# Optimization experiments

Measured on AMD Instinct MI355X. Metric: run time of the kernel, lower is better.

## Reference

```python
import jax, jax.numpy as jnp
import numpy as np

N_NODES = 1_000_000
N_EDGES = 5_000_000
N_GRAPHS = 4096
HIDDEN = 16


def transform(x):
    # Transform wrapper: fn=tanh, then nan_to_num(nan=0, posinf=10, neginf=-10).clamp(-10, 10)
    y = jnp.tanh(x)
    y = jnp.nan_to_num(y, nan=0.0, posinf=10.0, neginf=-10.0)
    return jnp.clip(y, -10.0, 10.0)


def setup_inputs() -> dict:
    key = jax.random.key(0)
    ks = jax.random.split(key, 10)
    x = jax.random.normal(ks[0], (N_NODES, 3), dtype=jnp.float32)
    edge_index = jax.random.randint(ks[1], (2, N_EDGES), 0, N_NODES, dtype=jnp.int32)
    batch = jnp.sort(jax.random.randint(ks[2], (N_NODES,), 0, N_GRAPHS, dtype=jnp.int32))
    s1 = 1.0 / np.sqrt(3.0)
    s2 = 1.0 / np.sqrt(HIDDEN)
    s3 = 1.0 / np.sqrt(2 * HIDDEN)
    w1 = jax.random.uniform(ks[3], (3, HIDDEN), jnp.float32, -s1, s1)
    b1 = jax.random.uniform(ks[4], (HIDDEN,), jnp.float32, -s1, s1)
    w2 = jax.random.uniform(ks[5], (HIDDEN, HIDDEN), jnp.float32, -s2, s2)
    b2 = jax.random.uniform(ks[6], (HIDDEN,), jnp.float32, -s2, s2)
    w3 = jax.random.uniform(ks[7], (2 * HIDDEN, 1), jnp.float32, -s3, s3)
    b3 = jax.random.uniform(ks[8], (1,), jnp.float32, -s3, s3)
    return {"x": x, "edge_index": edge_index, "batch": batch,
            "w1": w1, "b1": b1, "w2": w2, "b2": b2, "w3": w3, "b3": b3}


def reference(x, edge_index, batch, w1, b1, w2, b2, w3, b3):
    n_nodes = x.shape[0]
    h = transform(x @ w1 + b1)                                  # [N, H]
    row, col = edge_index[0], edge_index[1]
    # degree of each destination node (row), clamped to >= 1
    deg = jax.ops.segment_sum(jnp.ones((row.shape[0],), x.dtype), row,
                              num_segments=n_nodes)             # [N]
    deg = jnp.maximum(deg, 1.0)
    # gather source features, scatter-add to destinations, normalize
    agg = jax.ops.segment_sum(h[col], row, num_segments=n_nodes)  # [N, H]
    agg = agg / deg[:, None]
    h = transform(agg @ w2 + b2)                                # [N, H]
    # per-graph mean and max pooling
    cnt = jax.ops.segment_sum(jnp.ones((n_nodes,), x.dtype), batch,
                              num_segments=N_GRAPHS)            # [G]
    h_sum = jax.ops.segment_sum(h, batch, num_segments=N_GRAPHS)  # [G, H]
    h_mean = h_sum / jnp.maximum(cnt, 1.0)[:, None]
    h_max = jax.ops.segment_max(h, batch, num_segments=N_GRAPHS)  # [G, H]
    h_max = jnp.where(jnp.isneginf(h_max), 0.0, h_max)
    pooled = jnp.concatenate([h_mean, h_max], axis=1)           # [G, 2H]
    out = jax.nn.sigmoid(pooled @ w3 + b3)                      # [G, 1]
    return out.squeeze(-1)
```

## Files before the change

kernel.cpp:

```cpp
#include <hip/hip_runtime.h>
#include <hip/hip_bf16.h>
#include <hip/hip_fp16.h>

static constexpr int NN = 1000000;
static constexpr int NE = 5000000;
static constexpr int NG = 4096;
static constexpr int BIN_SH = 8;
static constexpr int BIN_SZ = 1 << BIN_SH;
static constexpr int NB = (NN + BIN_SZ - 1) >> BIN_SH;
static constexpr int CAP_SH = 11;
static constexpr int CAP = 1 << CAP_SH;
static constexpr int EPB = 16384;
static constexpr int BIN_BLOCKS = (NE + EPB - 1) / EPB;
static constexpr int CHUNK = 512;

__device__ __forceinline__ float fast_tanh(float x) {
    float e = __expf(2.0f * x);
    return 1.0f - 2.0f * __fdividef(1.0f, e + 1.0f);
}

__global__ __launch_bounds__(256) void x2h_k(
    const float* __restrict__ x, __half* __restrict__ xh)
{
    int i = blockIdx.x * 256 + threadIdx.x;
    if (i >= NN) return;
    union { __half2 h2[2]; uint2 u; } o;
    o.h2[0] = __floats2half2_rn(x[3 * i + 0], x[3 * i + 1]);
    o.h2[1] = __floats2half2_rn(x[3 * i + 2], 0.0f);
    *reinterpret_cast<uint2*>(xh + 4 * (size_t)i) = o.u;
}

__global__ __launch_bounds__(1024) void bin_scatter_k(
    const int* __restrict__ row, const int* __restrict__ col,
    int* __restrict__ binCursor, unsigned int* __restrict__ pack)
{
    __shared__ int hist[NB];
    for (int i = threadIdx.x; i < NB; i += 1024) hist[i] = 0;
    __syncthreads();
    int base = blockIdx.x * EPB;
#pragma unroll 4
    for (int k = 0; k < EPB / 1024; ++k) {
        int e = base + k * 1024 + threadIdx.x;
        if (e < NE) atomicAdd(&hist[row[e] >> BIN_SH], 1);
    }
    __syncthreads();
    for (int i = threadIdx.x; i < NB; i += 1024) {
        int c = hist[i];
        hist[i] = c ? ((i << CAP_SH) + atomicAdd(&binCursor[i], c)) : 0;
    }
    __syncthreads();
#pragma unroll 4
    for (int k = 0; k < EPB / 1024; ++k) {
        int e = base + k * 1024 + threadIdx.x;
        if (e >= NE) continue;
        int r = row[e];
        int c = col[e];
        int pos = atomicAdd(&hist[r >> BIN_SH], 1);
        pack[pos] = ((unsigned int)(r & (BIN_SZ - 1)) << 20) | (unsigned int)c;
    }
}

__global__ __launch_bounds__(256) void bucket_agg_k(
    const unsigned int* __restrict__ pack,
    const int* __restrict__ binCursor,
    const __half* __restrict__ xh,
    const int* __restrict__ batch,
    const float* __restrict__ w1,
    const float* __restrict__ b1,
    const float* __restrict__ w2,
    const float* __restrict__ b2,
    float* __restrict__ h_sum,
    unsigned int* __restrict__ h_max,
    int* __restrict__ cnt)
{
    __shared__ uint4 pay[CHUNK * 2];
    __shared__ int scnt[BIN_SZ];
    __shared__ int sstart[BIN_SZ];
    __shared__ int wsum[4];

    int tid = threadIdx.x;
    int lane = tid & 63, wid = tid >> 6;
    int b = blockIdx.x;
    int nodeBase = b << BIN_SH;
    int nNodes = min(BIN_SZ, NN - nodeBase);
    int es = b << CAP_SH;
    int ee = es + binCursor[b];

    __half2 acc8[8];
#pragma unroll
    for (int q = 0; q < 8; ++q) acc8[q] = __half2half2(__float2half(0.0f));
    int dg = 0;

    for (int cs = es; cs < ee; cs += CHUNK) {
        int m = min(CHUNK, ee - cs);
        scnt[tid] = 0;
        __syncthreads();

        uint2 gx[2];
        int rl2[2];
#pragma unroll
        for (int k = 0; k < 2; ++k) {
            int e = cs + k * 256 + tid;
            rl2[k] = -1;
            if (e < cs + m) {
                unsigned int p = pack[e];
                int c = (int)(p & 0xFFFFFu);
                rl2[k] = (int)(p >> 20);
                gx[k] = *reinterpret_cast<const uint2*>(xh + 4 * (size_t)c);
                atomicAdd(&scnt[rl2[k]], 1);
            }
        }
        __syncthreads();

        int v = scnt[tid];
        int sc = v;
#pragma unroll
        for (int off = 1; off < 64; off <<= 1) {
            int u = __shfl_up(sc, off);
            if (lane >= off) sc += u;
        }
        if (lane == 63) wsum[wid] = sc;
        __syncthreads();
        int pre = 0;
#pragma unroll
        for (int w = 0; w < 4; ++w) pre += (w < wid) ? wsum[w] : 0;
        int ex = pre + sc - v;
        sstart[tid] = ex;
        scnt[tid] = ex;
        __syncthreads();

#pragma unroll
        for (int k = 0; k < 2; ++k) {
            if (rl2[k] >= 0) {
                union { uint2 u; __half2 h2[2]; } xi;
                xi.u = gx[k];
                float2 x01 = __half22float2(xi.h2[0]);
                float x2v = __low2float(xi.h2[1]);
                union { __half2 h2[8]; uint4 u[2]; } o;
#pragma unroll
                for (int q = 0; q < 8; ++q) {
                    float va = fmaf(x2v, w1[32 + 2 * q], fmaf(x01.y, w1[16 + 2 * q],
                               fmaf(x01.x, w1[2 * q], b1[2 * q])));
                    float vb = fmaf(x2v, w1[33 + 2 * q], fmaf(x01.y, w1[17 + 2 * q],
                               fmaf(x01.x, w1[2 * q + 1], b1[2 * q + 1])));
                    o.h2[q] = __floats2half2_rn(fast_tanh(va), fast_tanh(vb));
                }
                int pos = atomicAdd(&scnt[rl2[k]], 1);
                pay[2 * pos + 0] = o.u[0];
                pay[2 * pos + 1] = o.u[1];
            }
        }
        __syncthreads();

        if (tid < nNodes) {
            int s0 = sstart[tid];
            int e0 = (tid < 255) ? sstart[tid + 1] : m;
            dg += e0 - s0;
            for (int e = s0; e < e0; ++e) {
                union { uint4 u; __half2 h2[4]; } ua, ub;
                ua.u = pay[2 * e + 0];
                ub.u = pay[2 * e + 1];
#pragma unroll
                for (int q = 0; q < 4; ++q) {
                    acc8[q] = __hadd2(acc8[q], ua.h2[q]);
                    acc8[4 + q] = __hadd2(acc8[4 + q], ub.h2[q]);
                }
            }
        }
        __syncthreads();
    }

    if (tid < nNodes) {
        float acc[16];
#pragma unroll
        for (int q = 0; q < 8; ++q) {
            float2 f = __half22float2(acc8[q]);
            acc[2 * q + 0] = f.x;
            acc[2 * q + 1] = f.y;
        }
        float inv = 1.0f / fmaxf((float)dg, 1.0f);
        float s[16];
#pragma unroll
        for (int j = 0; j < 16; ++j) s[j] = b2[j];
#pragma unroll
        for (int k = 0; k < 16; ++k) {
            float a = acc[k] * inv;
#pragma unroll
            for (int j = 0; j < 16; ++j) s[j] = fmaf(a, w2[16 * k + j], s[j]);
        }
        float m[16];
#pragma unroll
        for (int j = 0; j < 16; ++j) { s[j] = fast_tanh(s[j]); m[j] = s[j]; }

        int g = batch[nodeBase + tid];
        int gp = __shfl_up(g, 1);
        int head = (lane == 0) || (g != gp);
        unsigned long long hm = __ballot(head != 0);

        int f = head;
#pragma unroll
        for (int off = 1; off < 64; off <<= 1) {
            int fu = __shfl_up(f, off);
            bool take = (lane >= off) && (f == 0);
#pragma unroll
            for (int j = 0; j < 16; ++j) {
                float su = __shfl_up(s[j], off);
                float mu = __shfl_up(m[j], off);
                if (take) { s[j] += su; m[j] = fmaxf(m[j], mu); }
            }
            if (lane >= off) f |= fu;
        }

        int hnext = __shfl_down(head, 1);
        bool is_last = (lane == 63) || (hnext != 0);
        if (is_last) {
            unsigned long long below = hm & (~0ULL >> (63 - lane));
            int start = 63 - __clzll(below);
            int seglen = lane - start + 1;
#pragma unroll
            for (int j = 0; j < 16; ++j) {
                unsafeAtomicAdd(&h_sum[16 * g + j], s[j]);
                atomicMax(&h_max[16 * g + j], __float_as_uint(m[j] + 2.0f));
            }
            atomicAdd(&cnt[g], seglen);
        }
    }
}

__global__ __launch_bounds__(256) void out_k(
    const float* __restrict__ h_sum,
    const unsigned int* __restrict__ h_max,
    const int* __restrict__ cnt,
    const float* __restrict__ w3,
    const float* __restrict__ b3,
    float* __restrict__ out)
{
    int g = blockIdx.x * 256 + threadIdx.x;
    if (g >= NG) return;
    float invc = 1.0f / fmaxf((float)cnt[g], 1.0f);
    float acc = b3[0];
#pragma unroll
    for (int j = 0; j < 16; ++j) {
        float mean = h_sum[16 * g + j] * invc;
        unsigned int e = h_max[16 * g + j];
        float mx = (e == 0u) ? 0.0f : (__uint_as_float(e) - 2.0f);
        acc = fmaf(mean, w3[j], fmaf(mx, w3[16 + j], acc));
    }
    out[g] = 1.0f / (1.0f + __expf(-acc));
}

extern "C" void kernel_launch(void* const* d_in, const int* in_sizes, int n_in,
                              void* d_out, int out_size, void* d_ws, size_t ws_size,
                              hipStream_t stream)
{
    const float* x   = (const float*)d_in[0];
    const int*   ei  = (const int*)d_in[1];
    const int*   bat = (const int*)d_in[2];
    const float* w1  = (const float*)d_in[3];
    const float* b1  = (const float*)d_in[4];
    const float* w2  = (const float*)d_in[5];
    const float* b2  = (const float*)d_in[6];
    const float* w3  = (const float*)d_in[7];
    const float* b3  = (const float*)d_in[8];
    float* out = (float*)d_out;

    char* ws = (char*)d_ws;
    size_t off = 0;
    int* binCursor = (int*)(ws + off);         off += 16384;
    float* h_sum  = (float*)(ws + off);        off += (size_t)NG * 16 * 4;
    unsigned int* h_max = (unsigned int*)(ws + off); off += (size_t)NG * 16 * 4;
    int* cnt      = (int*)(ws + off);          off += (size_t)NG * 4;
    size_t zero_bytes = off;
    unsigned int* pack = (unsigned int*)(ws + off); off += (size_t)NB * CAP * 4;
    __half* xh    = (__half*)(ws + off);       off += (size_t)NN * 4 * 2;

    hipMemsetAsync(d_ws, 0, zero_bytes, stream);

    x2h_k<<<(NN + 255) / 256, 256, 0, stream>>>(x, xh);
    bin_scatter_k<<<BIN_BLOCKS, 1024, 0, stream>>>(ei, ei + NE, binCursor, pack);
    bucket_agg_k<<<NB, 256, 0, stream>>>(pack, binCursor, xh, bat,
                                         w1, b1, w2, b2, h_sum, h_max, cnt);
    out_k<<<(NG + 255) / 256, 256, 0, stream>>>(h_sum, h_max, cnt, w3, b3, out);
}
```

Measured before the change: 203.5 us.

## Prefetch next edge chunk in aggregation and batch loads in bin scatter

```diff
diff --git a/kernel.cpp b/kernel.cpp
--- a/kernel.cpp
+++ b/kernel.cpp
@@ -11,6 +11,7 @@
 static constexpr int CAP_SH = 11;
 static constexpr int CAP = 1 << CAP_SH;
 static constexpr int EPB = 16384;
+static constexpr int EPW = EPB / 1024;
 static constexpr int BIN_BLOCKS = (NE + EPB - 1) / EPB;
 static constexpr int CHUNK = 512;
 
@@ -38,26 +39,33 @@
     for (int i = threadIdx.x; i < NB; i += 1024) hist[i] = 0;
     __syncthreads();
     int base = blockIdx.x * EPB;
-#pragma unroll 4
-    for (int k = 0; k < EPB / 1024; ++k) {
+
+    int r[EPW], c[EPW];
+    bool val[EPW];
+#pragma unroll
+    for (int k = 0; k < EPW; ++k) {
         int e = base + k * 1024 + threadIdx.x;
-        if (e < NE) atomicAdd(&hist[row[e] >> BIN_SH], 1);
-    }
+        val[k] = e < NE;
+        r[k] = val[k] ? row[e] : 0;
+        c[k] = val[k] ? col[e] : 0;
+    }
+#pragma unroll
+    for (int k = 0; k < EPW; ++k)
+        if (val[k]) atomicAdd(&hist[r[k] >> BIN_SH], 1);
     __syncthreads();
     for (int i = threadIdx.x; i < NB; i += 1024) {
-        int c = hist[i];
-        hist[i] = c ? ((i << CAP_SH) + atomicAdd(&binCursor[i], c)) : 0;
+        int cc = hist[i];
+        hist[i] = cc ? ((i << CAP_SH) + atomicAdd(&binCursor[i], cc)) : 0;
     }
     __syncthreads();
-#pragma unroll 4
-    for (int k = 0; k < EPB / 1024; ++k) {
-        int e = base + k * 1024 + threadIdx.x;
-        if (e >= NE) continue;
-        int r = row[e];
-        int c = col[e];
-        int pos = atomicAdd(&hist[r >> BIN_SH], 1);
-        pack[pos] = ((unsigned int)(r & (BIN_SZ - 1)) << 20) | (unsigned int)c;
-    }
+    int pos[EPW];
+#pragma unroll
+    for (int k = 0; k < EPW; ++k)
+        if (val[k]) pos[k] = atomicAdd(&hist[r[k] >> BIN_SH], 1);
+#pragma unroll
+    for (int k = 0; k < EPW; ++k)
+        if (val[k]) pack[pos[k]] = ((unsigned int)(r[k] & (BIN_SZ - 1)) << 20)
+                                   | (unsigned int)c[k];
 }
 
 __global__ __launch_bounds__(256) void bucket_agg_k(
@@ -91,25 +99,29 @@
     for (int q = 0; q < 8; ++q) acc8[q] = __half2half2(__float2half(0.0f));
     int dg = 0;
 
+    uint2 gxA[2]; int rlA[2];
+    rlA[0] = rlA[1] = -1;
+    if (es < ee) {
+        int mm = min(CHUNK, ee - es);
+#pragma unroll
+        for (int k = 0; k < 2; ++k) {
+            int off = k * 256 + tid;
+            if (off < mm) {
+                unsigned int p = pack[es + off];
+                rlA[k] = (int)(p >> 20);
+                gxA[k] = *reinterpret_cast<const uint2*>(xh + 4 * (size_t)(p & 0xFFFFFu));
+            }
+        }
+    }
+
     for (int cs = es; cs < ee; cs += CHUNK) {
         int m = min(CHUNK, ee - cs);
         scnt[tid] = 0;
         __syncthreads();
 
-        uint2 gx[2];
-        int rl2[2];
-#pragma unroll
-        for (int k = 0; k < 2; ++k) {
-            int e = cs + k * 256 + tid;
-            rl2[k] = -1;
-            if (e < cs + m) {
-                unsigned int p = pack[e];
-                int c = (int)(p & 0xFFFFFu);
-                rl2[k] = (int)(p >> 20);
-                gx[k] = *reinterpret_cast<const uint2*>(xh + 4 * (size_t)c);
-                atomicAdd(&scnt[rl2[k]], 1);
-            }
-        }
+#pragma unroll
+        for (int k = 0; k < 2; ++k)
+            if (rlA[k] >= 0) atomicAdd(&scnt[rlA[k]], 1);
         __syncthreads();
 
         int v = scnt[tid];
@@ -131,9 +143,9 @@
 
 #pragma unroll
         for (int k = 0; k < 2; ++k) {
-            if (rl2[k] >= 0) {
+            if (rlA[k] >= 0) {
                 union { uint2 u; __half2 h2[2]; } xi;
-                xi.u = gx[k];
+                xi.u = gxA[k];
                 float2 x01 = __half22float2(xi.h2[0]);
                 float x2v = __low2float(xi.h2[1]);
                 union { __half2 h2[8]; uint4 u[2]; } o;
@@ -145,9 +157,24 @@
                                fmaf(x01.x, w1[2 * q + 1], b1[2 * q + 1])));
                     o.h2[q] = __floats2half2_rn(fast_tanh(va), fast_tanh(vb));
                 }
-                int pos = atomicAdd(&scnt[rl2[k]], 1);
+                int pos = atomicAdd(&scnt[rlA[k]], 1);
                 pay[2 * pos + 0] = o.u[0];
                 pay[2 * pos + 1] = o.u[1];
+            }
+        }
+
+        uint2 gxB[2]; int rlB[2];
+        rlB[0] = rlB[1] = -1;
+        if (cs + CHUNK < ee) {
+            int mm = min(CHUNK, ee - (cs + CHUNK));
+#pragma unroll
+            for (int k = 0; k < 2; ++k) {
+                int off = k * 256 + tid;
+                if (off < mm) {
+                    unsigned int p = pack[cs + CHUNK + off];
+                    rlB[k] = (int)(p >> 20);
+                    gxB[k] = *reinterpret_cast<const uint2*>(xh + 4 * (size_t)(p & 0xFFFFFu));
+                }
             }
         }
         __syncthreads();
@@ -168,6 +195,9 @@
             }
         }
         __syncthreads();
+
+#pragma unroll
+        for (int k = 0; k < 2; ++k) { gxA[k] = gxB[k]; rlA[k] = rlB[k]; }
     }
 
     if (tid < nNodes) {
```

Result: faster. 191.7 us (-5.8%).
